# Kernel optimization log

Measured on AMD Instinct MI355X. Metric: run time of the kernel, lower is better.

The kernel has to match this reference:

```python
import jax, jax.numpy as jnp
import numpy as np

# Conv2d_mvm config (matches init_kwargs): the bit-sliced crossbar MVM is a
# fixed-point emulation of an exact stride-1 conv2d with padding=1, no bias.
C_IN, C_OUT, K, H, W, PAD = 16, 16, 3, 1024, 1024, 1


def setup_inputs() -> dict:
    key = jax.random.key(0)
    kx, kw = jax.random.split(key)
    x = jax.random.normal(kx, (1, C_IN, H, W), dtype=jnp.float32)
    # kaiming_uniform-style init for the conv weight
    fan_in = C_IN * K * K
    bound = 1.0 / np.sqrt(fan_in)
    weight = jax.random.uniform(kw, (C_OUT, C_IN, K, K), dtype=jnp.float32,
                                minval=-bound, maxval=bound)
    return {"x": x, "weight": weight}


def reference(x, weight):
    # Ideal math of the bit-sliced crossbar MVM: per output pixel, the
    # flattened (C_in*K*K) receptive field dotted with each flattened filter.
    out = jax.lax.conv_general_dilated(
        x, weight,
        window_strides=(1, 1),
        padding=((PAD, PAD), (PAD, PAD)),
        dimension_numbers=("NCHW", "OIHW", "NCHW"),
    )
    # Original forward returns (C_out, H_out, W_out) with batch=1 assumed.
    return out[0]
```

## Files before the change

### kernel.cpp

```cpp
#include <hip/hip_runtime.h>


#define H 1024
#define W 1024
#define HW (H * W)
#define TW 128
#define TH 8
#define LROWS 10
#define NQ 34
#define NJOBS (LROWS * NQ)
#define LCOLS 130
#define LPITCH (LCOLS * 32)
#define LDS_BYTES (LROWS * LPITCH)

typedef __bf16 bf16x8 __attribute__((ext_vector_type(8)));
typedef float f32x4 __attribute__((ext_vector_type(4)));
typedef unsigned short ushort8 __attribute__((ext_vector_type(8)));
typedef unsigned int uint4v __attribute__((ext_vector_type(4)));

__device__ __host__ inline unsigned short f2bf(float f) {
  unsigned u = __builtin_bit_cast(unsigned, f);
  return (unsigned short)((u + 0x7fffu + ((u >> 16) & 1u)) >> 16);
}

__global__ __launch_bounds__(256) void conv_prep(const float* __restrict__ w,
                                                 unsigned short* __restrict__ wA) {
  int i = blockIdx.x * 256 + threadIdx.x;
  if (i >= 5 * 64 * 8) return;
  int j = i & 7;
  int l = (i >> 3) & 63;
  int p = i >> 9;
  int k = (l >> 4) * 8 + j;
  int t = 2 * p + (k >> 4);
  int ci = k & 15;
  int co = l & 15;
  float v = (t <= 8) ? w[co * 144 + ci * 9 + t] : 0.f;
  wA[i] = f2bf(v);
}

__device__ __forceinline__ void stage_job(int j, const float* __restrict__ x,
                                          int colbase, int rowbase, char* lds) {
  const int ly  = j / NQ;
  const int qx  = j - ly * NQ;
  const int gy  = rowbase - 1 + ly;
  const float rowm = ((unsigned)gy < (unsigned)H) ? 1.f : 0.f;
  const int gyc  = gy < 0 ? 0 : (gy > H - 1 ? H - 1 : gy);
  const int gx0  = colbase - 4 + 4 * qx;
  const int gx0c = gx0 < 0 ? 0 : (gx0 > W - 4 ? W - 4 : gx0);
  const float* xb = x + gyc * W + gx0c;

  f32x4 L[16];
#pragma unroll
  for (int c = 0; c < 16; ++c)
    L[c] = *(const f32x4*)(xb + c * HW);

#pragma unroll
  for (int i = 0; i < 4; ++i) {
    const int gx = gx0 + i;
    const int lx = gx - (colbase - 1);
    if ((unsigned)lx < (unsigned)LCOLS) {
      const float fm = rowm * (((unsigned)gx < (unsigned)W) ? 1.f : 0.f);
      const int lb = (ly * LPITCH + lx * 32) ^ (((lx >> 2) & 3) << 4);
#pragma unroll
      for (int h = 0; h < 2; ++h) {
        uint4v d;
#pragma unroll
        for (int p = 0; p < 4; ++p) {
          const unsigned lo = f2bf(L[h * 8 + 2 * p][i] * fm);
          const unsigned hi = f2bf(L[h * 8 + 2 * p + 1][i] * fm);
          d[p] = lo | (hi << 16);
        }
        *(uint4v*)(lds + (lb ^ (h << 4))) = d;
      }
    }
  }
}

__global__ __launch_bounds__(256, 3) void conv_mfma(
    const float* __restrict__ x, const unsigned short* __restrict__ wA,
    float* __restrict__ out) {
  __shared__ __align__(16) char lds[LDS_BYTES];

  const int tid  = threadIdx.x;
  const int lane = tid & 63;
  const int wave = tid >> 6;
  const int m = lane & 15;
  const int q = lane >> 4;
  const int colbase = blockIdx.x * TW;
  const int rowbase = blockIdx.y * TH;

  stage_job(tid, x, colbase, rowbase, lds);
  if (tid < NJOBS - 256) stage_job(256 + tid, x, colbase, rowbase, lds);

  ushort8 wU[5];
#pragma unroll
  for (int p = 0; p < 5; ++p)
    wU[p] = *(const ushort8*)&wA[(p * 64 + lane) * 8];

  int baseaddr[5];
#pragma unroll
  for (int p = 0; p < 5; ++p) {
    int t = 2 * p + (q >> 1);
    int ky = 0, kx = 0;
    if (t <= 8) { ky = t / 3; kx = t - ky * 3; }
    int col = m + kx;
    int b = ky * LPITCH + col * 32 + (q & 1) * 16;
    b ^= ((col >> 2) & 3) << 4;
    baseaddr[p] = b + wave * 2 * LPITCH;
  }

  __syncthreads();

#pragma unroll
  for (int r = 0; r < 2; ++r) {
#pragma unroll
    for (int g = 0; g < 8; ++g) {
      f32x4 acc = {0.f, 0.f, 0.f, 0.f};
#pragma unroll
      for (int p = 0; p < 5; ++p) {
        ushort8 bU = *(const ushort8*)(lds + (baseaddr[p] + r * LPITCH + g * 512));
        acc = __builtin_amdgcn_mfma_f32_16x16x32_bf16(
            __builtin_bit_cast(bf16x8, bU),
            __builtin_bit_cast(bf16x8, wU[p]),
            acc, 0, 0, 0);
      }
      const int y  = rowbase + wave * 2 + r;
      const int x0 = colbase + g * 16 + q * 4;
      *(f32x4*)(out + m * HW + y * W + x0) = acc;
    }
  }
}

extern "C" void kernel_launch(void* const* d_in, const int* in_sizes, int n_in,
                              void* d_out, int out_size, void* d_ws, size_t ws_size,
                              hipStream_t stream) {
  const float* x = (const float*)d_in[0];
  const float* w = (const float*)d_in[1];
  float* out = (float*)d_out;
  unsigned short* wA = (unsigned short*)d_ws;

  conv_prep<<<10, 256, 0, stream>>>(w, wA);

  dim3 grid(W / TW, H / TH);
  conv_mfma<<<grid, 256, 0, stream>>>(x, wA, out);
}
```

Measured before the change: 39.49 us.

## Halve tile height, use 512-thread blocks with per-half-channel staging and nontemporal stores

Shrinks the output tile to 4 rows with 512 threads per block, so each staging thread loads only 8 input channels and each wave computes 4 column groups of one row. The aim is more blocks and waves in flight to hide global-load latency, plus nontemporal output stores to avoid polluting cache. The cost is more halo rows re-read relative to useful output (6 loaded rows for 4 output rows instead of 10 for 8), and the launch bound of 8 blocks of 512 threads may constrain registers.

```diff
diff --git a/kernel.cpp b/kernel.cpp
--- a/kernel.cpp
+++ b/kernel.cpp
@@ -5,8 +5,8 @@
 #define W 1024
 #define HW (H * W)
 #define TW 128
-#define TH 8
-#define LROWS 10
+#define TH 4
+#define LROWS 6
 #define NQ 34
 #define NJOBS (LROWS * NQ)
 #define LCOLS 130
@@ -38,45 +38,7 @@
   wA[i] = f2bf(v);
 }
 
-__device__ __forceinline__ void stage_job(int j, const float* __restrict__ x,
-                                          int colbase, int rowbase, char* lds) {
-  const int ly  = j / NQ;
-  const int qx  = j - ly * NQ;
-  const int gy  = rowbase - 1 + ly;
-  const float rowm = ((unsigned)gy < (unsigned)H) ? 1.f : 0.f;
-  const int gyc  = gy < 0 ? 0 : (gy > H - 1 ? H - 1 : gy);
-  const int gx0  = colbase - 4 + 4 * qx;
-  const int gx0c = gx0 < 0 ? 0 : (gx0 > W - 4 ? W - 4 : gx0);
-  const float* xb = x + gyc * W + gx0c;
-
-  f32x4 L[16];
-#pragma unroll
-  for (int c = 0; c < 16; ++c)
-    L[c] = *(const f32x4*)(xb + c * HW);
-
-#pragma unroll
-  for (int i = 0; i < 4; ++i) {
-    const int gx = gx0 + i;
-    const int lx = gx - (colbase - 1);
-    if ((unsigned)lx < (unsigned)LCOLS) {
-      const float fm = rowm * (((unsigned)gx < (unsigned)W) ? 1.f : 0.f);
-      const int lb = (ly * LPITCH + lx * 32) ^ (((lx >> 2) & 3) << 4);
-#pragma unroll
-      for (int h = 0; h < 2; ++h) {
-        uint4v d;
-#pragma unroll
-        for (int p = 0; p < 4; ++p) {
-          const unsigned lo = f2bf(L[h * 8 + 2 * p][i] * fm);
-          const unsigned hi = f2bf(L[h * 8 + 2 * p + 1][i] * fm);
-          d[p] = lo | (hi << 16);
-        }
-        *(uint4v*)(lds + (lb ^ (h << 4))) = d;
-      }
-    }
-  }
-}
-
-__global__ __launch_bounds__(256, 3) void conv_mfma(
+__global__ __launch_bounds__(512, 8) void conv_mfma(
     const float* __restrict__ x, const unsigned short* __restrict__ wA,
     float* __restrict__ out) {
   __shared__ __align__(16) char lds[LDS_BYTES];
@@ -89,14 +51,49 @@
   const int colbase = blockIdx.x * TW;
   const int rowbase = blockIdx.y * TH;
 
-  stage_job(tid, x, colbase, rowbase, lds);
-  if (tid < NJOBS - 256) stage_job(256 + tid, x, colbase, rowbase, lds);
+  if (tid < 2 * NJOBS) {
+    const int hf = tid & 1;
+    const int j  = tid >> 1;
+    const int ly = j / NQ;
+    const int qx = j - ly * NQ;
+    const int gy = rowbase - 1 + ly;
+    const float rowm = ((unsigned)gy < (unsigned)H) ? 1.f : 0.f;
+    const int gyc  = gy < 0 ? 0 : (gy > H - 1 ? H - 1 : gy);
+    const int gx0  = colbase - 4 + 4 * qx;
+    const int gx0c = gx0 < 0 ? 0 : (gx0 > W - 4 ? W - 4 : gx0);
+    const float* xb = x + hf * 8 * HW + gyc * W + gx0c;
+
+    f32x4 L[8];
+#pragma unroll
+    for (int c = 0; c < 8; ++c)
+      L[c] = *(const f32x4*)(xb + c * HW);
+
+#pragma unroll
+    for (int i = 0; i < 4; ++i) {
+      const int gx = gx0 + i;
+      const int lx = gx - (colbase - 1);
+      if ((unsigned)lx < (unsigned)LCOLS) {
+        const float fm = rowm * (((unsigned)gx < (unsigned)W) ? 1.f : 0.f);
+        const int lb = (ly * LPITCH + lx * 32) ^ (((lx >> 2) & 3) << 4);
+        uint4v d;
+#pragma unroll
+        for (int p = 0; p < 4; ++p) {
+          const unsigned lo = f2bf(L[2 * p][i] * fm);
+          const unsigned hi = f2bf(L[2 * p + 1][i] * fm);
+          d[p] = lo | (hi << 16);
+        }
+        *(uint4v*)(lds + (lb ^ (hf << 4))) = d;
+      }
+    }
+  }
 
   ushort8 wU[5];
 #pragma unroll
   for (int p = 0; p < 5; ++p)
     wU[p] = *(const ushort8*)&wA[(p * 64 + lane) * 8];
 
+  const int r = wave >> 1;
+  const int gbase = (wave & 1) * 4;
   int baseaddr[5];
 #pragma unroll
   for (int p = 0; p < 5; ++p) {
@@ -106,28 +103,25 @@
     int col = m + kx;
     int b = ky * LPITCH + col * 32 + (q & 1) * 16;
     b ^= ((col >> 2) & 3) << 4;
-    baseaddr[p] = b + wave * 2 * LPITCH;
+    baseaddr[p] = b + r * LPITCH;
   }
 
   __syncthreads();
 
 #pragma unroll
-  for (int r = 0; r < 2; ++r) {
+  for (int g = 0; g < 4; ++g) {
+    f32x4 acc = {0.f, 0.f, 0.f, 0.f};
 #pragma unroll
-    for (int g = 0; g < 8; ++g) {
-      f32x4 acc = {0.f, 0.f, 0.f, 0.f};
-#pragma unroll
-      for (int p = 0; p < 5; ++p) {
-        ushort8 bU = *(const ushort8*)(lds + (baseaddr[p] + r * LPITCH + g * 512));
-        acc = __builtin_amdgcn_mfma_f32_16x16x32_bf16(
-            __builtin_bit_cast(bf16x8, bU),
-            __builtin_bit_cast(bf16x8, wU[p]),
-            acc, 0, 0, 0);
-      }
-      const int y  = rowbase + wave * 2 + r;
-      const int x0 = colbase + g * 16 + q * 4;
-      *(f32x4*)(out + m * HW + y * W + x0) = acc;
+    for (int p = 0; p < 5; ++p) {
+      ushort8 bU = *(const ushort8*)(lds + (baseaddr[p] + (gbase + g) * 512));
+      acc = __builtin_amdgcn_mfma_f32_16x16x32_bf16(
+          __builtin_bit_cast(bf16x8, bU),
+          __builtin_bit_cast(bf16x8, wU[p]),
+          acc, 0, 0, 0);
     }
+    const int y  = rowbase + r;
+    const int x0 = colbase + (gbase + g) * 16 + q * 4;
+    __builtin_nontemporal_store(acc, (f32x4*)(out + m * HW + y * W + x0));
   }
 }
 
@@ -142,5 +136,5 @@
   conv_prep<<<10, 256, 0, stream>>>(w, wA);
 
   dim3 grid(W / TW, H / TH);
-  conv_mfma<<<grid, 256, 0, stream>>>(x, wA, out);
+  conv_mfma<<<grid, 512, 0, stream>>>(x, wA, out);
 }
```

After: 41.94 us. 1.06x slower.

## Halve tile height and split channel staging across waves for higher occupancy

Applied to the files above, without the earlier changes.

Reduces the output tile from 8 to 4 rows, so LDS shrinks to 6 halo rows and each wave computes one output row. Staging is reorganised so that each wave loads only 8 of the 16 input channels for two jobs, which cuts per-thread register use. Launch bounds rise to 6 blocks per CU. The aim is higher occupancy to hide global-load latency, at the cost of more halo reloads (6 rows staged per 4 output rows instead of 10 per 8).

```diff
diff --git a/kernel.cpp b/kernel.cpp
--- a/kernel.cpp
+++ b/kernel.cpp
@@ -5,10 +5,11 @@
 #define W 1024
 #define HW (H * W)
 #define TW 128
-#define TH 8
-#define LROWS 10
+#define TH 4
+#define LROWS 6
 #define NQ 34
 #define NJOBS (LROWS * NQ)
+#define NHALF 102
 #define LCOLS 130
 #define LPITCH (LCOLS * 32)
 #define LDS_BYTES (LROWS * LPITCH)
@@ -38,45 +39,7 @@
   wA[i] = f2bf(v);
 }
 
-__device__ __forceinline__ void stage_job(int j, const float* __restrict__ x,
-                                          int colbase, int rowbase, char* lds) {
-  const int ly  = j / NQ;
-  const int qx  = j - ly * NQ;
-  const int gy  = rowbase - 1 + ly;
-  const float rowm = ((unsigned)gy < (unsigned)H) ? 1.f : 0.f;
-  const int gyc  = gy < 0 ? 0 : (gy > H - 1 ? H - 1 : gy);
-  const int gx0  = colbase - 4 + 4 * qx;
-  const int gx0c = gx0 < 0 ? 0 : (gx0 > W - 4 ? W - 4 : gx0);
-  const float* xb = x + gyc * W + gx0c;
-
-  f32x4 L[16];
-#pragma unroll
-  for (int c = 0; c < 16; ++c)
-    L[c] = *(const f32x4*)(xb + c * HW);
-
-#pragma unroll
-  for (int i = 0; i < 4; ++i) {
-    const int gx = gx0 + i;
-    const int lx = gx - (colbase - 1);
-    if ((unsigned)lx < (unsigned)LCOLS) {
-      const float fm = rowm * (((unsigned)gx < (unsigned)W) ? 1.f : 0.f);
-      const int lb = (ly * LPITCH + lx * 32) ^ (((lx >> 2) & 3) << 4);
-#pragma unroll
-      for (int h = 0; h < 2; ++h) {
-        uint4v d;
-#pragma unroll
-        for (int p = 0; p < 4; ++p) {
-          const unsigned lo = f2bf(L[h * 8 + 2 * p][i] * fm);
-          const unsigned hi = f2bf(L[h * 8 + 2 * p + 1][i] * fm);
-          d[p] = lo | (hi << 16);
-        }
-        *(uint4v*)(lds + (lb ^ (h << 4))) = d;
-      }
-    }
-  }
-}
-
-__global__ __launch_bounds__(256, 3) void conv_mfma(
+__global__ __launch_bounds__(256, 6) void conv_mfma(
     const float* __restrict__ x, const unsigned short* __restrict__ wA,
     float* __restrict__ out) {
   __shared__ __align__(16) char lds[LDS_BYTES];
@@ -89,8 +52,61 @@
   const int colbase = blockIdx.x * TW;
   const int rowbase = blockIdx.y * TH;
 
-  stage_job(tid, x, colbase, rowbase, lds);
-  if (tid < NJOBS - 256) stage_job(256 + tid, x, colbase, rowbase, lds);
+  const int phalf = wave & 1;
+  const int qhalf = wave >> 1;
+  int lyk[2], gx0k[2];
+  float rowmk[2];
+  unsigned voffk[2];
+  bool actk[2];
+#pragma unroll
+  for (int k = 0; k < 2; ++k) {
+    const int jj = k * 64 + lane;
+    actk[k] = jj < NHALF;
+    const int j = qhalf * NHALF + (actk[k] ? jj : NHALF - 1);
+    const int ly = j / NQ, qx = j - ly * NQ;
+    lyk[k] = ly;
+    const int gy = rowbase - 1 + ly;
+    rowmk[k] = ((unsigned)gy < (unsigned)H) ? 1.f : 0.f;
+    const int gyc = gy < 0 ? 0 : (gy > H - 1 ? H - 1 : gy);
+    const int gx0 = colbase - 4 + 4 * qx;
+    gx0k[k] = gx0;
+    const int gx0c = gx0 < 0 ? 0 : (gx0 > W - 4 ? W - 4 : gx0);
+    voffk[k] = (unsigned)(gyc * W + gx0c);
+  }
+
+  f32x4 L[8][2];
+#pragma unroll
+  for (int c = 0; c < 8; ++c) {
+    const float* xp = x + (phalf * 8 + c) * HW;
+    L[c][0] = *(const f32x4*)(xp + voffk[0]);
+    L[c][1] = *(const f32x4*)(xp + voffk[1]);
+    __builtin_amdgcn_sched_barrier(0);
+  }
+
+#pragma unroll
+  for (int k = 0; k < 2; ++k) {
+    if (actk[k]) {
+#pragma unroll
+      for (int i = 0; i < 4; ++i) {
+        const int gx = gx0k[k] + i;
+        const int lx = gx - (colbase - 1);
+        if ((unsigned)lx < (unsigned)LCOLS) {
+          const float fm = rowmk[k] * (((unsigned)gx < (unsigned)W) ? 1.f : 0.f);
+          uint4v d;
+#pragma unroll
+          for (int p = 0; p < 4; ++p) {
+            const unsigned lo = f2bf(L[2 * p][k][i] * fm);
+            const unsigned hi = f2bf(L[2 * p + 1][k][i] * fm);
+            d[p] = lo | (hi << 16);
+          }
+          const int b =
+              (lyk[k] * LPITCH + lx * 32 + phalf * 16) ^ (((lx >> 2) & 3) << 4);
+          *(uint4v*)(lds + b) = d;
+        }
+      }
+    }
+  }
+  __builtin_amdgcn_sched_barrier(0);
 
   ushort8 wU[5];
 #pragma unroll
@@ -106,28 +122,25 @@
     int col = m + kx;
     int b = ky * LPITCH + col * 32 + (q & 1) * 16;
     b ^= ((col >> 2) & 3) << 4;
-    baseaddr[p] = b + wave * 2 * LPITCH;
+    baseaddr[p] = b + wave * LPITCH;
   }
 
   __syncthreads();
 
 #pragma unroll
-  for (int r = 0; r < 2; ++r) {
+  for (int g = 0; g < 8; ++g) {
+    f32x4 acc = {0.f, 0.f, 0.f, 0.f};
 #pragma unroll
-    for (int g = 0; g < 8; ++g) {
-      f32x4 acc = {0.f, 0.f, 0.f, 0.f};
-#pragma unroll
-      for (int p = 0; p < 5; ++p) {
-        ushort8 bU = *(const ushort8*)(lds + (baseaddr[p] + r * LPITCH + g * 512));
-        acc = __builtin_amdgcn_mfma_f32_16x16x32_bf16(
-            __builtin_bit_cast(bf16x8, bU),
-            __builtin_bit_cast(bf16x8, wU[p]),
-            acc, 0, 0, 0);
-      }
-      const int y  = rowbase + wave * 2 + r;
-      const int x0 = colbase + g * 16 + q * 4;
-      *(f32x4*)(out + m * HW + y * W + x0) = acc;
+    for (int p = 0; p < 5; ++p) {
+      ushort8 bU = *(const ushort8*)(lds + (baseaddr[p] + g * 512));
+      acc = __builtin_amdgcn_mfma_f32_16x16x32_bf16(
+          __builtin_bit_cast(bf16x8, bU),
+          __builtin_bit_cast(bf16x8, wU[p]),
+          acc, 0, 0, 0);
     }
+    const int y  = rowbase + wave;
+    const int x0 = colbase + g * 16 + q * 4;
+    *(f32x4*)(out + m * HW + y * W + x0) = acc;
   }
 }
 
```

New measurement: 41.29 us. +4.5%, slower.

## Use 1024-thread blocks with 16-row tiles and one output row per wave

Applied to the files above, without the earlier changes.

Doubles the tile height to 16 rows, so 18 staged rows serve 16 output rows instead of 10 serving 8, which cuts halo re-reads of the input. Blocks grow to 1024 threads (16 waves) and each wave computes one output row. Staging is done in a single pass by 612 threads, loading channels in two halves of 8 to lower register pressure. This raises LDS use per block and means fewer, larger blocks, which could hurt occupancy or tail balance.

```diff
diff --git a/kernel.cpp b/kernel.cpp
--- a/kernel.cpp
+++ b/kernel.cpp
@@ -5,8 +5,8 @@
 #define W 1024
 #define HW (H * W)
 #define TW 128
-#define TH 8
-#define LROWS 10
+#define TH 16
+#define LROWS 18
 #define NQ 34
 #define NJOBS (LROWS * NQ)
 #define LCOLS 130
@@ -38,45 +38,7 @@
   wA[i] = f2bf(v);
 }
 
-__device__ __forceinline__ void stage_job(int j, const float* __restrict__ x,
-                                          int colbase, int rowbase, char* lds) {
-  const int ly  = j / NQ;
-  const int qx  = j - ly * NQ;
-  const int gy  = rowbase - 1 + ly;
-  const float rowm = ((unsigned)gy < (unsigned)H) ? 1.f : 0.f;
-  const int gyc  = gy < 0 ? 0 : (gy > H - 1 ? H - 1 : gy);
-  const int gx0  = colbase - 4 + 4 * qx;
-  const int gx0c = gx0 < 0 ? 0 : (gx0 > W - 4 ? W - 4 : gx0);
-  const float* xb = x + gyc * W + gx0c;
-
-  f32x4 L[16];
-#pragma unroll
-  for (int c = 0; c < 16; ++c)
-    L[c] = *(const f32x4*)(xb + c * HW);
-
-#pragma unroll
-  for (int i = 0; i < 4; ++i) {
-    const int gx = gx0 + i;
-    const int lx = gx - (colbase - 1);
-    if ((unsigned)lx < (unsigned)LCOLS) {
-      const float fm = rowm * (((unsigned)gx < (unsigned)W) ? 1.f : 0.f);
-      const int lb = (ly * LPITCH + lx * 32) ^ (((lx >> 2) & 3) << 4);
-#pragma unroll
-      for (int h = 0; h < 2; ++h) {
-        uint4v d;
-#pragma unroll
-        for (int p = 0; p < 4; ++p) {
-          const unsigned lo = f2bf(L[h * 8 + 2 * p][i] * fm);
-          const unsigned hi = f2bf(L[h * 8 + 2 * p + 1][i] * fm);
-          d[p] = lo | (hi << 16);
-        }
-        *(uint4v*)(lds + (lb ^ (h << 4))) = d;
-      }
-    }
-  }
-}
-
-__global__ __launch_bounds__(256, 3) void conv_mfma(
+__global__ __launch_bounds__(1024, 8) void conv_mfma(
     const float* __restrict__ x, const unsigned short* __restrict__ wA,
     float* __restrict__ out) {
   __shared__ __align__(16) char lds[LDS_BYTES];
@@ -89,8 +51,47 @@
   const int colbase = blockIdx.x * TW;
   const int rowbase = blockIdx.y * TH;
 
-  stage_job(tid, x, colbase, rowbase, lds);
-  if (tid < NJOBS - 256) stage_job(256 + tid, x, colbase, rowbase, lds);
+  if (tid < NJOBS) {
+    const int ly  = tid / NQ;
+    const int qx  = tid - ly * NQ;
+    const int gy  = rowbase - 1 + ly;
+    const float rowm = ((unsigned)gy < (unsigned)H) ? 1.f : 0.f;
+    const int gyc  = gy < 0 ? 0 : (gy > H - 1 ? H - 1 : gy);
+    const int gx0  = colbase - 4 + 4 * qx;
+    const int gx0c = gx0 < 0 ? 0 : (gx0 > W - 4 ? W - 4 : gx0);
+    const float* xb = x + gyc * W + gx0c;
+
+    float fm[4];
+    int lok[4], lb[4];
+#pragma unroll
+    for (int i = 0; i < 4; ++i) {
+      const int gx = gx0 + i;
+      fm[i] = rowm * (((unsigned)gx < (unsigned)W) ? 1.f : 0.f);
+      const int lx = gx - (colbase - 1);
+      lok[i] = (unsigned)lx < (unsigned)LCOLS;
+      lb[i]  = (ly * LPITCH + lx * 32) ^ (((lx >> 2) & 3) << 4);
+    }
+#pragma unroll
+    for (int h = 0; h < 2; ++h) {
+      f32x4 L[8];
+#pragma unroll
+      for (int c = 0; c < 8; ++c)
+        L[c] = *(const f32x4*)(xb + (h * 8 + c) * HW);
+#pragma unroll
+      for (int i = 0; i < 4; ++i) {
+        if (lok[i]) {
+          uint4v d;
+#pragma unroll
+          for (int p = 0; p < 4; ++p) {
+            const unsigned lo = f2bf(L[2 * p][i] * fm[i]);
+            const unsigned hi = f2bf(L[2 * p + 1][i] * fm[i]);
+            d[p] = lo | (hi << 16);
+          }
+          *(uint4v*)(lds + (lb[i] ^ (h << 4))) = d;
+        }
+      }
+    }
+  }
 
   ushort8 wU[5];
 #pragma unroll
@@ -106,28 +107,25 @@
     int col = m + kx;
     int b = ky * LPITCH + col * 32 + (q & 1) * 16;
     b ^= ((col >> 2) & 3) << 4;
-    baseaddr[p] = b + wave * 2 * LPITCH;
+    baseaddr[p] = b + wave * LPITCH;
   }
 
   __syncthreads();
 
 #pragma unroll
-  for (int r = 0; r < 2; ++r) {
+  for (int g = 0; g < 8; ++g) {
+    f32x4 acc = {0.f, 0.f, 0.f, 0.f};
 #pragma unroll
-    for (int g = 0; g < 8; ++g) {
-      f32x4 acc = {0.f, 0.f, 0.f, 0.f};
-#pragma unroll
-      for (int p = 0; p < 5; ++p) {
-        ushort8 bU = *(const ushort8*)(lds + (baseaddr[p] + r * LPITCH + g * 512));
-        acc = __builtin_amdgcn_mfma_f32_16x16x32_bf16(
-            __builtin_bit_cast(bf16x8, bU),
-            __builtin_bit_cast(bf16x8, wU[p]),
-            acc, 0, 0, 0);
-      }
-      const int y  = rowbase + wave * 2 + r;
-      const int x0 = colbase + g * 16 + q * 4;
-      *(f32x4*)(out + m * HW + y * W + x0) = acc;
+    for (int p = 0; p < 5; ++p) {
+      ushort8 bU = *(const ushort8*)(lds + (baseaddr[p] + g * 512));
+      acc = __builtin_amdgcn_mfma_f32_16x16x32_bf16(
+          __builtin_bit_cast(bf16x8, bU),
+          __builtin_bit_cast(bf16x8, wU[p]),
+          acc, 0, 0, 0);
     }
+    const int y  = rowbase + wave;
+    const int x0 = colbase + g * 16 + q * 4;
+    *(f32x4*)(out + m * HW + y * W + x0) = acc;
   }
 }
 
@@ -142,5 +140,5 @@
   conv_prep<<<10, 256, 0, stream>>>(w, wA);
 
   dim3 grid(W / TW, H / TH);
-  conv_mfma<<<grid, 256, 0, stream>>>(x, wA, out);
+  conv_mfma<<<grid, 1024, 0, stream>>>(x, wA, out);
 }
```

Result: faster. 36.85 us (-6.7%).
